# Optimization experiments

Hardware: AMD Instinct MI355X
Metric: run time of the kernel (lower is better)

The kernel has to match this reference:

```python
import jax, jax.numpy as jnp
import numpy as np

S, L, K = 4, 256, 32          # num_states, seq length, neighbors
ORIG_H, EMB_H, EXV, RANK = 128, 256, 384, 16


def _integrate(x, Wq, Wk, seq_idx, emb_idx, hidden, rank):
    """AttentionIntegrator.forward: QK^T softmax -> double mean -> softmax -> weighted pool of raw x."""
    x = jnp.moveaxis(x, (seq_idx, emb_idx), (-2, -1))
    orig_shape = x.shape
    Ls = orig_shape[-2]
    xf = x.reshape(-1, Ls, hidden)               # (B, Ls, hidden)
    B = xf.shape[0]
    q = (xf @ Wq.T).reshape(B, Ls, rank, hidden)  # head_dim == hidden
    k = (xf @ Wk.T).reshape(B, Ls, rank, hidden)
    scale = 1.0 / jnp.sqrt(jnp.asarray(hidden, xf.dtype))
    scores = jnp.einsum('blhd,bmhd->bhlm', q, k) * scale
    attn = jax.nn.softmax(scores, axis=-1)        # (B, rank, Ls, Ls)
    w = jax.nn.softmax(attn.mean(axis=(1, 2)), axis=-1)  # (B, Ls)
    pooled = jnp.einsum('bl,bld->bd', w, xf)      # (B, hidden)
    return (pooled.reshape(*orig_shape[:-2], hidden),
            w.reshape(*orig_shape[:-2], Ls))


def setup_inputs() -> dict:
    key = jax.random.key(0)
    ks = jax.random.split(key, 12)
    sc = lambda fan_in: 1.0 / np.sqrt(fan_in)
    return {
        'h_V':    jax.random.normal(ks[0], (S, L, ORIG_H), jnp.float32),
        'h_EXV':  jax.random.normal(ks[1], (S, L, K, EXV), jnp.float32),
        'W_hV':   jax.random.normal(ks[2], (EMB_H, ORIG_H), jnp.float32) * sc(ORIG_H),
        'b_hV':   jnp.zeros((EMB_H,), jnp.float32),
        'Wq_hv':  jax.random.normal(ks[3], (RANK * EMB_H, EMB_H), jnp.float32) * sc(EMB_H),
        'Wk_hv':  jax.random.normal(ks[4], (RANK * EMB_H, EMB_H), jnp.float32) * sc(EMB_H),
        'Wq_ce':  jax.random.normal(ks[5], (RANK * EXV, EXV), jnp.float32) * sc(EXV),
        'Wk_ce':  jax.random.normal(ks[6], (RANK * EXV, EXV), jnp.float32) * sc(EXV),
        'W_ce':   jax.random.normal(ks[7], (EMB_H, EXV), jnp.float32) * sc(EXV),
        'b_ce':   jnp.zeros((EMB_H,), jnp.float32),
        'Wq_sce': jax.random.normal(ks[8], (RANK * EMB_H, EMB_H), jnp.float32) * sc(EMB_H),
        'Wk_sce': jax.random.normal(ks[9], (RANK * EMB_H, EMB_H), jnp.float32) * sc(EMB_H),
    }


def reference(h_V, h_EXV, W_hV, b_hV, Wq_hv, Wk_hv, Wq_ce, Wk_ce, W_ce, b_ce, Wq_sce, Wk_sce):
    # diffmodel.get_weights
    hv = h_V @ W_hV.T + b_hV                                  # (S, L, EMB_H)
    h_V_int, h_V_w = _integrate(hv, Wq_hv, Wk_hv, 0, 2, EMB_H, RANK)   # pool over states
    # chemical environment: pool over k neighbors per (state, position)
    ce, _local_w = _integrate(h_EXV, Wq_ce, Wk_ce, 2, 3, EXV, RANK)    # (S, L, EXV)
    ce = ce @ W_ce.T + b_ce                                   # (S, L, EMB_H)
    ce_int, ce_w = _integrate(ce, Wq_sce, Wk_sce, 0, 2, EMB_H, RANK)   # pool over states
    return (h_V_int[None], h_V_w[None], ce_int[None], ce_w[None])
```

## Files before the change

kernel.cpp:

```cpp
#include <hip/hip_runtime.h>

typedef _Float16 f16;
typedef _Float16 f16x8 __attribute__((ext_vector_type(8)));
typedef _Float16 f16x4 __attribute__((ext_vector_type(4)));
typedef float f32x4 __attribute__((ext_vector_type(4)));

#define MFMA16(a, b, c) __builtin_amdgcn_mfma_f32_16x16x32_f16(a, b, c, 0, 0, 0)
#define MFMA16K16(a, b, c) __builtin_amdgcn_mfma_f32_16x16x16f16(a, b, c, 0, 0, 0)

__global__ __launch_bounds__(256) void k_mt(const float* __restrict__ Wq,
                                            const float* __restrict__ Wk,
                                            f16* __restrict__ MT, int H) {
    const int h = blockIdx.x;
    const int ntile = H >> 6;
    const int nkk = H >> 5;
    const int frow = (blockIdx.y / ntile) * 64;
    const int ecol = (blockIdx.y % ntile) * 64;
    const int t = threadIdx.x;
    const int lane = t & 63;
    const int w = t >> 6;
    const int wr = w >> 1, wc = w & 1;

    __shared__ __align__(16) f16 As[64][40];
    __shared__ __align__(16) f16 Ks[64][40];

    f32x4 acc[2][2] = {};
    const int d = t >> 3;
    const int e8 = (t & 7) * 8;

    for (int kk = 0; kk < nkk; ++kk) {
        const float* gq = Wq + (size_t)(h * H + kk * 32 + d) * H + ecol + e8;
        const float* gk = Wk + (size_t)(h * H + kk * 32 + d) * H + frow + e8;
        float q[8], k[8];
#pragma unroll
        for (int i = 0; i < 8; ++i) { q[i] = gq[i]; k[i] = gk[i]; }
        __syncthreads();
#pragma unroll
        for (int i = 0; i < 8; ++i) { As[e8 + i][d] = (f16)q[i]; Ks[e8 + i][d] = (f16)k[i]; }
        __syncthreads();
        f16x8 a[2], b[2];
#pragma unroll
        for (int rt = 0; rt < 2; ++rt)
            a[rt] = *(const f16x8*)&Ks[wr * 32 + rt * 16 + (lane & 15)][(lane >> 4) * 8];
#pragma unroll
        for (int nt = 0; nt < 2; ++nt)
            b[nt] = *(const f16x8*)&As[wc * 32 + nt * 16 + (lane & 15)][(lane >> 4) * 8];
#pragma unroll
        for (int rt = 0; rt < 2; ++rt)
#pragma unroll
            for (int nt = 0; nt < 2; ++nt)
                acc[rt][nt] = MFMA16(a[rt], b[nt], acc[rt][nt]);
    }
#pragma unroll
    for (int rt = 0; rt < 2; ++rt)
#pragma unroll
        for (int nt = 0; nt < 2; ++nt)
#pragma unroll
            for (int j = 0; j < 4; ++j) {
                int f = frow + wr * 32 + rt * 16 + (lane >> 4) * 4 + j;
                int e = ecol + wc * 32 + nt * 16 + (lane & 15);
                MT[(((size_t)h * nkk + (e >> 5)) * H + f) * 32 + (e & 31)] = (f16)acc[rt][nt][j];
            }
}

__global__ __launch_bounds__(256) void k_lin(const float* __restrict__ in,
                                             const float* __restrict__ W,
                                             const float* __restrict__ bias,
                                             float* __restrict__ out, int K) {
    const int t = threadIdx.x;
    const int r0 = blockIdx.x * 4;
    __shared__ float ins[4][384];
    __shared__ float Ws[256][33];
#pragma unroll
    for (int r = 0; r < 4; ++r)
        for (int off = t; off < K; off += 256)
            ins[r][off] = in[(size_t)(r0 + r) * K + off];
    float acc[4] = {};
    for (int d0 = 0; d0 < K; d0 += 32) {
        __syncthreads();
        for (int i = t; i < 256 * 32; i += 256) {
            int j = i >> 5, dd = i & 31;
            Ws[j][dd] = W[(size_t)j * K + d0 + dd];
        }
        __syncthreads();
#pragma unroll 8
        for (int dd = 0; dd < 32; ++dd) {
            float wv = Ws[t][dd];
#pragma unroll
            for (int r = 0; r < 4; ++r) acc[r] += wv * ins[r][d0 + dd];
        }
    }
    float bv = bias[t];
#pragma unroll
    for (int r = 0; r < 4; ++r) out[(size_t)(r0 + r) * 256 + t] = acc[r] + bv;
}

__global__ __launch_bounds__(256) void k_small_int(const float* __restrict__ X,
                                                   const f16* __restrict__ MT,
                                                   float* __restrict__ wpart) {
    const int t = threadIdx.x;
    const int lane = t & 63;
    const int w = t >> 6;
    const int g = lane >> 4;
    const int l15 = lane & 15;
    const int pos0 = blockIdx.x * 4;
    const int h = blockIdx.y;

    __shared__ __align__(16) f16 Xs[16][264];
    __shared__ __align__(16) f16 Ts[16][264];

    {
        int row = t >> 4, d0 = (t & 15) * 16;
        int s = row & 3, p = row >> 2;
        const float* gx = X + (size_t)(s * 256 + pos0 + p) * 256 + d0;
#pragma unroll
        for (int i = 0; i < 16; i += 8) {
            float4 v0 = *(const float4*)(gx + i);
            float4 v1 = *(const float4*)(gx + i + 4);
            f16x8 o;
            o[0] = (f16)v0.x; o[1] = (f16)v0.y; o[2] = (f16)v0.z; o[3] = (f16)v0.w;
            o[4] = (f16)v1.x; o[5] = (f16)v1.y; o[6] = (f16)v1.z; o[7] = (f16)v1.w;
            *(f16x8*)&Xs[row][d0 + i] = o;
        }
    }
    __syncthreads();

    const f16* mh = MT + (size_t)h * 8 * 256 * 32;
    const int fb = w * 64 + l15;
    f32x4 acc[4] = {};
    f16x8 bq[4], bn[4];
#pragma unroll
    for (int nt = 0; nt < 4; ++nt)
        bq[nt] = *(const f16x8*)(mh + (size_t)(fb + nt * 16) * 32 + g * 8);
#pragma unroll
    for (int kk = 0; kk < 8; ++kk) {
        if (kk < 7) {
#pragma unroll
            for (int nt = 0; nt < 4; ++nt)
                bn[nt] = *(const f16x8*)(mh + ((size_t)(kk + 1) * 256 + fb + nt * 16) * 32 + g * 8);
        }
        f16x8 a = *(const f16x8*)&Xs[l15][kk * 32 + g * 8];
#pragma unroll
        for (int nt = 0; nt < 4; ++nt) acc[nt] = MFMA16(a, bq[nt], acc[nt]);
#pragma unroll
        for (int nt = 0; nt < 4; ++nt) bq[nt] = bn[nt];
    }
#pragma unroll
    for (int nt = 0; nt < 4; ++nt)
#pragma unroll
        for (int j = 0; j < 4; ++j)
            Ts[g * 4 + j][w * 64 + nt * 16 + l15] = (f16)acc[nt][j];
    __syncthreads();

    f32x4 sacc = {};
#pragma unroll
    for (int ks = 0; ks < 8; ++ks) {
        f16x8 a = *(const f16x8*)&Ts[l15][ks * 32 + g * 8];
        f16x8 b = *(const f16x8*)&Xs[l15][ks * 32 + g * 8];
        sacc = MFMA16(a, b, sacc);
    }
    if (w == 0 && (l15 >> 2) == g) {
        const float scale = 1.0f / 16.0f;
        float add = 0.f;
#pragma unroll
        for (int j = 0; j < 4; ++j) {
            float v = sacc[j] * scale;
            float m = v;
            m = fmaxf(m, __shfl_xor(m, 1));
            m = fmaxf(m, __shfl_xor(m, 2));
            float e = expf(v - m);
            float s2 = e;
            s2 += __shfl_xor(s2, 1);
            s2 += __shfl_xor(s2, 2);
            add += e / s2;
        }
        int pg = pos0 + g;
        wpart[((size_t)h * 256 + pg) * 4 + (l15 & 3)] = add;
    }
}

__global__ __launch_bounds__(256) void k_small_fin(const float* __restrict__ wpart,
                                                   const float* __restrict__ X,
                                                   float* __restrict__ out_int,
                                                   float* __restrict__ out_w) {
    const int pos = blockIdx.x, t = threadIdx.x;
    __shared__ float red[64];
    __shared__ float ws[4];
    if (t < 64) red[t] = wpart[((size_t)(t >> 2) * 256 + pos) * 4 + (t & 3)];
    __syncthreads();
    if (t == 0) {
        float v[4];
#pragma unroll
        for (int s = 0; s < 4; ++s) {
            float x = 0.f;
            for (int hh = 0; hh < 16; ++hh) x += red[hh * 4 + s];
            v[s] = x * (1.0f / 64.0f);
        }
        float m = fmaxf(fmaxf(v[0], v[1]), fmaxf(v[2], v[3]));
        float sum = 0.f;
#pragma unroll
        for (int s = 0; s < 4; ++s) { v[s] = expf(v[s] - m); sum += v[s]; }
#pragma unroll
        for (int s = 0; s < 4; ++s) ws[s] = v[s] / sum;
    }
    __syncthreads();
    if (t < 4) out_w[pos * 4 + t] = ws[t];
    float v = 0.f;
#pragma unroll
    for (int s = 0; s < 4; ++s) v += ws[s] * X[(size_t)(s * 256 + pos) * 256 + t];
    out_int[(size_t)pos * 256 + t] = v;
}

#define PART_OFF 49152

__global__ __launch_bounds__(256, 2) void k_ce_int(const float* __restrict__ Xg32,
                                                   const f16* __restrict__ MT,
                                                   float* __restrict__ acc_out) {
    const int t = threadIdx.x;
    const int lane = t & 63;
    const int w = t >> 6;
    const int g = lane >> 4;
    const int l15 = lane & 15;
    const int bg = blockIdx.x;

    extern __shared__ __align__(16) char smem[];

    {
        const float* xg = Xg32 + (size_t)bg * 64 * 384;
#pragma unroll
        for (int p = 0; p < 12; ++p) {
            int idx = p * 256 + t;
            int row = idx / 48, s = idx - row * 48;
            int c = s ^ (row & 7);
            const float* src = xg + row * 384 + c * 8;
            float4 v0 = *(const float4*)src;
            float4 v1 = *(const float4*)(src + 4);
            f16x8 o;
            o[0] = (f16)v0.x; o[1] = (f16)v0.y; o[2] = (f16)v0.z; o[3] = (f16)v0.w;
            o[4] = (f16)v1.x; o[5] = (f16)v1.y; o[6] = (f16)v1.z; o[7] = (f16)v1.w;
            *(f16x8*)(smem + idx * 16) = o;
        }
    }
    __syncthreads();

    const f16* mall = MT;
    const int frow = w * 96 + l15;

    f16x8 A[3][6];
#pragma unroll
    for (int ft = 0; ft < 6; ++ft) {
        A[0][ft] = *(const f16x8*)(mall + ((size_t)0 * 384 + frow + ft * 16) * 32 + g * 8);
        A[1][ft] = *(const f16x8*)(mall + ((size_t)1 * 384 + frow + ft * 16) * 32 + g * 8);
    }

    for (int hi = 0; hi < 16; ++hi) {
        f32x4 acc[6][4] = {};
#pragma unroll
        for (int kk = 0; kk < 12; ++kk) {
            {
                int step = hi * 12 + kk + 2;
                int ns = step < 192 ? step : 191;
#pragma unroll
                for (int ft = 0; ft < 6; ++ft)
                    A[(kk + 2) % 3][ft] =
                        *(const f16x8*)(mall + ((size_t)ns * 384 + frow + ft * 16) * 32 + g * 8);
            }
            f16x8 xb[4];
#pragma unroll
            for (int mt = 0; mt < 4; ++mt) {
                int row = mt * 16 + l15;
                int ch = kk * 4 + g;
                xb[mt] = *(const f16x8*)(smem + row * 768 + ((ch ^ (row & 7)) << 4));
            }
            __builtin_amdgcn_s_setprio(1);
#pragma unroll
            for (int ft = 0; ft < 6; ++ft)
#pragma unroll
                for (int mt = 0; mt < 4; ++mt)
                    acc[ft][mt] = MFMA16(A[kk % 3][ft], xb[mt], acc[ft][mt]);
            __builtin_amdgcn_s_setprio(0);
        }

        f16x4 bf[6][4];
#pragma unroll
        for (int ft = 0; ft < 6; ++ft)
#pragma unroll
            for (int mt = 0; mt < 4; ++mt) {
                f32x4 v = acc[ft][mt];
                f16x4 o;
                o[0] = (f16)v[0]; o[1] = (f16)v[1]; o[2] = (f16)v[2]; o[3] = (f16)v[3];
                bf[ft][mt] = o;
            }

        f32x4 s2[2][2][2] = {};
#pragma unroll
        for (int b = 0; b < 2; ++b)
#pragma unroll
            for (int ks = 0; ks < 6; ++ks)
#pragma unroll
                for (int it = 0; it < 2; ++it) {
                    int r = b * 32 + it * 16 + l15;
                    int ch = 12 * w + 2 * ks + (g >> 1);
                    f16x4 av = *(const f16x4*)(smem + r * 768 + ((ch ^ (r & 7)) << 4) + 8 * (g & 1));
#pragma unroll
                    for (int lt = 0; lt < 2; ++lt)
                        s2[b][it][lt] = MFMA16K16(av, bf[ks][2 * b + lt], s2[b][it][lt]);
                }

#pragma unroll
        for (int b = 0; b < 2; ++b)
#pragma unroll
            for (int lt = 0; lt < 2; ++lt) {
                int dst = b * 2 + lt;
                if (dst != w) {
                    int src = w - (w > dst ? 1 : 0);
#pragma unroll
                    for (int it = 0; it < 2; ++it)
                        *(f32x4*)(smem + PART_OFF + (((dst * 3 + src) * 2 + it) << 10) + lane * 16) =
                            s2[b][it][lt];
                }
            }
        __syncthreads();

        {
            const int b = w >> 1, lt = w & 1;
            f32x4 own0, own1;
            if (w == 0)      { own0 = s2[0][0][0]; own1 = s2[0][1][0]; }
            else if (w == 1) { own0 = s2[0][0][1]; own1 = s2[0][1][1]; }
            else if (w == 2) { own0 = s2[1][0][0]; own1 = s2[1][1][0]; }
            else             { own0 = s2[1][0][1]; own1 = s2[1][1][1]; }
            f32x4 ssum[2] = { own0, own1 };
#pragma unroll
            for (int src = 0; src < 3; ++src)
#pragma unroll
                for (int it = 0; it < 2; ++it)
                    ssum[it] += *(const f32x4*)(smem + PART_OFF + (((w * 3 + src) * 2 + it) << 10) + lane * 16);

            const float scale = 0.051031036307982884f;
            float mx = -1e30f;
#pragma unroll
            for (int it = 0; it < 2; ++it)
#pragma unroll
                for (int j = 0; j < 4; ++j) mx = fmaxf(mx, ssum[it][j] * scale);
            mx = fmaxf(mx, __shfl_xor(mx, 16));
            mx = fmaxf(mx, __shfl_xor(mx, 32));
            float e[2][4];
            float den = 0.f;
#pragma unroll
            for (int it = 0; it < 2; ++it)
#pragma unroll
                for (int j = 0; j < 4; ++j) {
                    e[it][j] = expf(ssum[it][j] * scale - mx);
                    den += e[it][j];
                }
            den += __shfl_xor(den, 16);
            den += __shfl_xor(den, 32);
            float inv = 1.f / den;
            float cs[2][4];
#pragma unroll
            for (int it = 0; it < 2; ++it)
#pragma unroll
                for (int j = 0; j < 4; ++j) {
                    float v = e[it][j] * inv;
                    v += __shfl_xor(v, 1);
                    v += __shfl_xor(v, 2);
                    v += __shfl_xor(v, 4);
                    v += __shfl_xor(v, 8);
                    cs[it][j] = v;
                }
            if (l15 == 0) {
                float* o = acc_out + (((size_t)hi * 1024 + bg * 2 + b) * 2 + lt) * 32;
#pragma unroll
                for (int it = 0; it < 2; ++it)
#pragma unroll
                    for (int j = 0; j < 4; ++j)
                        o[it * 16 + g * 4 + j] = cs[it][j];
            }
        }
        __syncthreads();
    }
}

__global__ __launch_bounds__(128) void k_ce_pool(const float* __restrict__ accp,
                                                 const float* __restrict__ exv,
                                                 float* __restrict__ pooled) {
    const int b = blockIdx.x;
    const int t = threadIdx.x;
    __shared__ float wm[32];
    __shared__ float ww[32];
    if (t < 32) {
        float s = 0.f;
#pragma unroll
        for (int h = 0; h < 16; ++h) {
            s += accp[(((size_t)h * 1024 + b) * 2 + 0) * 32 + t];
            s += accp[(((size_t)h * 1024 + b) * 2 + 1) * 32 + t];
        }
        wm[t] = s * (1.0f / 512.0f);
    }
    __syncthreads();
    if (t == 0) {
        float m = wm[0];
        for (int i = 1; i < 32; ++i) m = fmaxf(m, wm[i]);
        float s = 0.f;
        for (int i = 0; i < 32; ++i) { float e = expf(wm[i] - m); ww[i] = e; s += e; }
        float inv = 1.f / s;
        for (int i = 0; i < 32; ++i) ww[i] *= inv;
    }
    __syncthreads();
    for (int d = t; d < 384; d += 128) {
        float v = 0.f;
#pragma unroll
        for (int m = 0; m < 32; ++m) v += ww[m] * exv[((size_t)b * 32 + m) * 384 + d];
        pooled[(size_t)b * 384 + d] = v;
    }
}

extern "C" void kernel_launch(void* const* d_in, const int* in_sizes, int n_in,
                              void* d_out, int out_size, void* d_ws, size_t ws_size,
                              hipStream_t stream) {
    const float* h_V    = (const float*)d_in[0];
    const float* h_EXV  = (const float*)d_in[1];
    const float* W_hV   = (const float*)d_in[2];
    const float* b_hV   = (const float*)d_in[3];
    const float* Wq_hv  = (const float*)d_in[4];
    const float* Wk_hv  = (const float*)d_in[5];
    const float* Wq_ce  = (const float*)d_in[6];
    const float* Wk_ce  = (const float*)d_in[7];
    const float* W_ce   = (const float*)d_in[8];
    const float* b_ce   = (const float*)d_in[9];
    const float* Wq_sce = (const float*)d_in[10];
    const float* Wk_sce = (const float*)d_in[11];
    float* out = (float*)d_out;

    char* ws = (char*)d_ws;
    f16*   mt_hv  = (f16*)(ws + 0);
    f16*   mt_sce = (f16*)(ws + 2097152);
    f16*   mt_ce  = (f16*)(ws + 4194304);
    float* hv     = (float*)(ws + 8912896);
    float* ce     = (float*)(ws + 9961472);
    float* accp   = (float*)(ws + 11010048);
    float* pooled = (float*)(ws + 15204352);
    float* wpart  = accp;

    k_mt<<<dim3(16, 16), 256, 0, stream>>>(Wq_hv, Wk_hv, mt_hv, 256);
    k_mt<<<dim3(16, 36), 256, 0, stream>>>(Wq_ce, Wk_ce, mt_ce, 384);
    k_mt<<<dim3(16, 16), 256, 0, stream>>>(Wq_sce, Wk_sce, mt_sce, 256);
    k_lin<<<256, 256, 0, stream>>>(h_V, W_hV, b_hV, hv, 128);
    k_small_int<<<dim3(64, 16), 256, 0, stream>>>(hv, mt_hv, wpart);
    k_small_fin<<<256, 256, 0, stream>>>(wpart, hv, out + 0, out + 65536);
    k_ce_int<<<dim3(512), 256, 73728, stream>>>(h_EXV, mt_ce, accp);
    k_ce_pool<<<1024, 128, 0, stream>>>(accp, h_EXV, pooled);
    k_lin<<<256, 256, 0, stream>>>(pooled, W_ce, b_ce, ce, 384);
    k_small_int<<<dim3(64, 16), 256, 0, stream>>>(ce, mt_sce, wpart);
    k_small_fin<<<256, 256, 0, stream>>>(wpart, ce, out + 66560, out + 132096);
}
```

Baseline: 315.3 us.

## Split k_ce_int work across eight waves with tree reduction of score partials

The main neighbor-attention kernel now runs 512 threads per block instead of 256. Each wave handles 48 feature rows instead of 96, and the MT prefetch ring shrinks from triple to double buffering, which lowers per-wave register pressure and raises waves in flight. The cross-wave reduction of score partials becomes a staged pairwise exchange through shared memory, and the softmax reductions are split across wave pairs. This adds many more __syncthreads per head iteration, and the shorter prefetch distance may expose global load latency.

Measured after the change: 351.9 us. +11.6%, slower.

```diff
diff --git a/kernel.cpp b/kernel.cpp
--- a/kernel.cpp
+++ b/kernel.cpp
@@ -211,9 +211,9 @@
     out_int[(size_t)pos * 256 + t] = v;
 }
 
-#define PART_OFF 49152
-
-__global__ __launch_bounds__(256, 2) void k_ce_int(const float* __restrict__ Xg32,
+#define EX_OFF 49152
+
+__global__ __launch_bounds__(512, 2) void k_ce_int(const float* __restrict__ Xg32,
                                                    const f16* __restrict__ MT,
                                                    float* __restrict__ acc_out) {
     const int t = threadIdx.x;
@@ -224,12 +224,13 @@
     const int bg = blockIdx.x;
 
     extern __shared__ __align__(16) char smem[];
+    char* EX = smem + EX_OFF;
 
     {
         const float* xg = Xg32 + (size_t)bg * 64 * 384;
 #pragma unroll
-        for (int p = 0; p < 12; ++p) {
-            int idx = p * 256 + t;
+        for (int p = 0; p < 6; ++p) {
+            int idx = p * 512 + t;
             int row = idx / 48, s = idx - row * 48;
             int c = s ^ (row & 7);
             const float* src = xg + row * 384 + c * 8;
@@ -244,46 +245,42 @@
     __syncthreads();
 
     const f16* mall = MT;
-    const int frow = w * 96 + l15;
-
-    f16x8 A[3][6];
-#pragma unroll
-    for (int ft = 0; ft < 6; ++ft) {
-        A[0][ft] = *(const f16x8*)(mall + ((size_t)0 * 384 + frow + ft * 16) * 32 + g * 8);
-        A[1][ft] = *(const f16x8*)(mall + ((size_t)1 * 384 + frow + ft * 16) * 32 + g * 8);
-    }
+    const int frow = w * 48 + l15;
+
+    f16x8 A[2][3];
+#pragma unroll
+    for (int ft = 0; ft < 3; ++ft)
+        A[0][ft] = *(const f16x8*)(mall + (size_t)(frow + ft * 16) * 32 + g * 8);
 
     for (int hi = 0; hi < 16; ++hi) {
-        f32x4 acc[6][4] = {};
+        f32x4 acc[3][4] = {};
 #pragma unroll
         for (int kk = 0; kk < 12; ++kk) {
             {
-                int step = hi * 12 + kk + 2;
+                int step = hi * 12 + kk + 1;
                 int ns = step < 192 ? step : 191;
 #pragma unroll
-                for (int ft = 0; ft < 6; ++ft)
-                    A[(kk + 2) % 3][ft] =
-                        *(const f16x8*)(mall + ((size_t)ns * 384 + frow + ft * 16) * 32 + g * 8);
+                for (int ft = 0; ft < 3; ++ft)
+                    A[(kk + 1) & 1][ft] =
+                        *(const f16x8*)(mall + (size_t)ns * 12288 + (size_t)(frow + ft * 16) * 32 + g * 8);
             }
+            const int xaddr = l15 * 768 + (((kk * 4 + g) ^ (l15 & 7)) << 4);
             f16x8 xb[4];
 #pragma unroll
-            for (int mt = 0; mt < 4; ++mt) {
-                int row = mt * 16 + l15;
-                int ch = kk * 4 + g;
-                xb[mt] = *(const f16x8*)(smem + row * 768 + ((ch ^ (row & 7)) << 4));
-            }
+            for (int mt = 0; mt < 4; ++mt)
+                xb[mt] = *(const f16x8*)(smem + xaddr + mt * 12288);
             __builtin_amdgcn_s_setprio(1);
 #pragma unroll
-            for (int ft = 0; ft < 6; ++ft)
+            for (int ft = 0; ft < 3; ++ft)
 #pragma unroll
                 for (int mt = 0; mt < 4; ++mt)
-                    acc[ft][mt] = MFMA16(A[kk % 3][ft], xb[mt], acc[ft][mt]);
+                    acc[ft][mt] = MFMA16(A[kk & 1][ft], xb[mt], acc[ft][mt]);
             __builtin_amdgcn_s_setprio(0);
         }
 
-        f16x4 bf[6][4];
-#pragma unroll
-        for (int ft = 0; ft < 6; ++ft)
+        f16x4 bf[3][4];
+#pragma unroll
+        for (int ft = 0; ft < 3; ++ft)
 #pragma unroll
             for (int mt = 0; mt < 4; ++mt) {
                 f32x4 v = acc[ft][mt];
@@ -296,85 +293,109 @@
 #pragma unroll
         for (int b = 0; b < 2; ++b)
 #pragma unroll
-            for (int ks = 0; ks < 6; ++ks)
+            for (int ks = 0; ks < 3; ++ks)
 #pragma unroll
                 for (int it = 0; it < 2; ++it) {
-                    int r = b * 32 + it * 16 + l15;
-                    int ch = 12 * w + 2 * ks + (g >> 1);
-                    f16x4 av = *(const f16x4*)(smem + r * 768 + ((ch ^ (r & 7)) << 4) + 8 * (g & 1));
+                    int ch = 6 * w + 2 * ks + (g >> 1);
+                    int av_addr = b * 24576 + it * 12288 + l15 * 768 +
+                                  ((ch ^ (l15 & 7)) << 4) + 8 * (g & 1);
+                    f16x4 av = *(const f16x4*)(smem + av_addr);
 #pragma unroll
                     for (int lt = 0; lt < 2; ++lt)
-                        s2[b][it][lt] = MFMA16K16(av, bf[ks][2 * b + lt], s2[b][it][lt]);
+                        s2[b][it][lt] = MFMA16K16(av, bf[ks][b * 2 + lt], s2[b][it][lt]);
                 }
 
-#pragma unroll
-        for (int b = 0; b < 2; ++b)
-#pragma unroll
-            for (int lt = 0; lt < 2; ++lt) {
-                int dst = b * 2 + lt;
-                if (dst != w) {
-                    int src = w - (w > dst ? 1 : 0);
-#pragma unroll
-                    for (int it = 0; it < 2; ++it)
-                        *(f32x4*)(smem + PART_OFF + (((dst * 3 + src) * 2 + it) << 10) + lane * 16) =
-                            s2[b][it][lt];
-                }
+        f32x4 p00, p01, p10, p11;
+        if (w >= 4) {
+            char* dst = EX + (w - 4) * 4096 + lane * 16;
+            *(f32x4*)(dst) = s2[0][0][0];
+            *(f32x4*)(dst + 1024) = s2[0][0][1];
+            *(f32x4*)(dst + 2048) = s2[0][1][0];
+            *(f32x4*)(dst + 3072) = s2[0][1][1];
+        }
+        __syncthreads();
+        if (w < 4) {
+            const char* pb = EX + w * 4096 + lane * 16;
+            p00 = s2[0][0][0] + *(const f32x4*)(pb);
+            p01 = s2[0][0][1] + *(const f32x4*)(pb + 1024);
+            p10 = s2[0][1][0] + *(const f32x4*)(pb + 2048);
+            p11 = s2[0][1][1] + *(const f32x4*)(pb + 3072);
+            char* dst = EX + w * 4096 + lane * 16;
+            *(f32x4*)(dst) = s2[1][0][0];
+            *(f32x4*)(dst + 1024) = s2[1][0][1];
+            *(f32x4*)(dst + 2048) = s2[1][1][0];
+            *(f32x4*)(dst + 3072) = s2[1][1][1];
+        }
+        __syncthreads();
+        if (w >= 4) {
+            const char* pb = EX + (w - 4) * 4096 + lane * 16;
+            p00 = s2[1][0][0] + *(const f32x4*)(pb);
+            p01 = s2[1][0][1] + *(const f32x4*)(pb + 1024);
+            p10 = s2[1][1][0] + *(const f32x4*)(pb + 2048);
+            p11 = s2[1][1][1] + *(const f32x4*)(pb + 3072);
+        }
+        __syncthreads();
+
+        {
+            char* dst = EX + w * 2048 + lane * 16;
+            if ((w & 2) == 0) { *(f32x4*)dst = p10; *(f32x4*)(dst + 1024) = p11; }
+            else              { *(f32x4*)dst = p00; *(f32x4*)(dst + 1024) = p01; }
+        }
+        __syncthreads();
+        f32x4 q0, q1;
+        {
+            const char* pb = EX + (w ^ 2) * 2048 + lane * 16;
+            if ((w & 2) == 0) { q0 = p00 + *(const f32x4*)pb; q1 = p01 + *(const f32x4*)(pb + 1024); }
+            else              { q0 = p10 + *(const f32x4*)pb; q1 = p11 + *(const f32x4*)(pb + 1024); }
+        }
+        __syncthreads();
+
+        {
+            char* dst = EX + w * 1024 + lane * 16;
+            if ((w & 1) == 0) *(f32x4*)dst = q1;
+            else              *(f32x4*)dst = q0;
+        }
+        __syncthreads();
+        f32x4 fin;
+        {
+            const char* pb = EX + (w ^ 1) * 1024 + lane * 16;
+            if ((w & 1) == 0) fin = q0 + *(const f32x4*)pb;
+            else              fin = q1 + *(const f32x4*)pb;
+        }
+        __syncthreads();
+
+        {
+            const float scale = 0.051031036307982884f;
+            float v0 = fin[0] * scale, v1 = fin[1] * scale;
+            float v2 = fin[2] * scale, v3 = fin[3] * scale;
+            float lm = fmaxf(fmaxf(v0, v1), fmaxf(v2, v3));
+            lm = fmaxf(lm, __shfl_xor(lm, 16));
+            lm = fmaxf(lm, __shfl_xor(lm, 32));
+            if (lane < 16) *(float*)(EX + w * 64 + lane * 4) = lm;
+            __syncthreads();
+            float m = fmaxf(lm, *(const float*)(EX + (w ^ 2) * 64 + l15 * 4));
+            float e0 = expf(v0 - m), e1 = expf(v1 - m);
+            float e2 = expf(v2 - m), e3 = expf(v3 - m);
+            float ls = e0 + e1 + e2 + e3;
+            ls += __shfl_xor(ls, 16);
+            ls += __shfl_xor(ls, 32);
+            if (lane < 16) *(float*)(EX + 512 + w * 64 + lane * 4) = ls;
+            __syncthreads();
+            float den = ls + *(const float*)(EX + 512 + (w ^ 2) * 64 + l15 * 4);
+            float inv = 1.f / den;
+            float r0 = e0 * inv, r1 = e1 * inv, r2 = e2 * inv, r3 = e3 * inv;
+#pragma unroll
+            for (int d = 1; d < 16; d <<= 1) {
+                r0 += __shfl_xor(r0, d);
+                r1 += __shfl_xor(r1, d);
+                r2 += __shfl_xor(r2, d);
+                r3 += __shfl_xor(r3, d);
             }
-        __syncthreads();
-
-        {
-            const int b = w >> 1, lt = w & 1;
-            f32x4 own0, own1;
-            if (w == 0)      { own0 = s2[0][0][0]; own1 = s2[0][1][0]; }
-            else if (w == 1) { own0 = s2[0][0][1]; own1 = s2[0][1][1]; }
-            else if (w == 2) { own0 = s2[1][0][0]; own1 = s2[1][1][0]; }
-            else             { own0 = s2[1][0][1]; own1 = s2[1][1][1]; }
-            f32x4 ssum[2] = { own0, own1 };
-#pragma unroll
-            for (int src = 0; src < 3; ++src)
-#pragma unroll
-                for (int it = 0; it < 2; ++it)
-                    ssum[it] += *(const f32x4*)(smem + PART_OFF + (((w * 3 + src) * 2 + it) << 10) + lane * 16);
-
-            const float scale = 0.051031036307982884f;
-            float mx = -1e30f;
-#pragma unroll
-            for (int it = 0; it < 2; ++it)
-#pragma unroll
-                for (int j = 0; j < 4; ++j) mx = fmaxf(mx, ssum[it][j] * scale);
-            mx = fmaxf(mx, __shfl_xor(mx, 16));
-            mx = fmaxf(mx, __shfl_xor(mx, 32));
-            float e[2][4];
-            float den = 0.f;
-#pragma unroll
-            for (int it = 0; it < 2; ++it)
-#pragma unroll
-                for (int j = 0; j < 4; ++j) {
-                    e[it][j] = expf(ssum[it][j] * scale - mx);
-                    den += e[it][j];
-                }
-            den += __shfl_xor(den, 16);
-            den += __shfl_xor(den, 32);
-            float inv = 1.f / den;
-            float cs[2][4];
-#pragma unroll
-            for (int it = 0; it < 2; ++it)
-#pragma unroll
-                for (int j = 0; j < 4; ++j) {
-                    float v = e[it][j] * inv;
-                    v += __shfl_xor(v, 1);
-                    v += __shfl_xor(v, 2);
-                    v += __shfl_xor(v, 4);
-                    v += __shfl_xor(v, 8);
-                    cs[it][j] = v;
-                }
             if (l15 == 0) {
-                float* o = acc_out + (((size_t)hi * 1024 + bg * 2 + b) * 2 + lt) * 32;
-#pragma unroll
-                for (int it = 0; it < 2; ++it)
-#pragma unroll
-                    for (int j = 0; j < 4; ++j)
-                        o[it * 16 + g * 4 + j] = cs[it][j];
+                const int ob = w >> 2, oit = (w >> 1) & 1, olt = w & 1;
+                float* o = acc_out + (((size_t)hi * 1024 + bg * 2 + ob) * 2 + olt) * 32 +
+                           oit * 16 + g * 4;
+                o[0] = r0; o[1] = r1; o[2] = r2; o[3] = r3;
             }
         }
         __syncthreads();
@@ -448,7 +469,7 @@
     k_lin<<<256, 256, 0, stream>>>(h_V, W_hV, b_hV, hv, 128);
     k_small_int<<<dim3(64, 16), 256, 0, stream>>>(hv, mt_hv, wpart);
     k_small_fin<<<256, 256, 0, stream>>>(wpart, hv, out + 0, out + 65536);
-    k_ce_int<<<dim3(512), 256, 73728, stream>>>(h_EXV, mt_ce, accp);
+    k_ce_int<<<dim3(512), 512, 65536, stream>>>(h_EXV, mt_ce, accp);
     k_ce_pool<<<1024, 128, 0, stream>>>(accp, h_EXV, pooled);
     k_lin<<<256, 256, 0, stream>>>(pooled, W_ce, b_ce, ce, 384);
     k_small_int<<<dim3(64, 16), 256, 0, stream>>>(ce, mt_sce, wpart);
```

## Double rows per block in ce integrator to halve per-row weight fetches

Applied to the files above, without the earlier changes.

k_ce_int now uses 512-thread blocks that each process 128 neighbor rows instead of 64. Each of 8 waves covers 48 feature rows of the combined Q/K matrix against 8 row tiles, so each fetched weight fragment is reused across twice as many rows and global/L2 traffic for MT drops. The cross-wave score reduction moves to a 64KB LDS buffer and runs in two rounds, each with a synchronisation, where four waves reduce and compute the softmax. The 160KB LDS footprint allows only one block per CU, and the larger register tiles may reduce occupancy.

New measurement: 318.7 us. About the same (+1.1%).

```diff
diff --git a/kernel.cpp b/kernel.cpp
--- a/kernel.cpp
+++ b/kernel.cpp
@@ -211,9 +211,9 @@
     out_int[(size_t)pos * 256 + t] = v;
 }
 
-#define PART_OFF 49152
-
-__global__ __launch_bounds__(256, 2) void k_ce_int(const float* __restrict__ Xg32,
+#define BUF_OFF 98304
+
+__global__ __launch_bounds__(512, 2) void k_ce_int(const float* __restrict__ Xg32,
                                                    const f16* __restrict__ MT,
                                                    float* __restrict__ acc_out) {
     const int t = threadIdx.x;
@@ -224,12 +224,13 @@
     const int bg = blockIdx.x;
 
     extern __shared__ __align__(16) char smem[];
+    char* BUF = smem + BUF_OFF;
 
     {
-        const float* xg = Xg32 + (size_t)bg * 64 * 384;
+        const float* xg = Xg32 + (size_t)bg * 128 * 384;
 #pragma unroll
         for (int p = 0; p < 12; ++p) {
-            int idx = p * 256 + t;
+            int idx = p * 512 + t;
             int row = idx / 48, s = idx - row * 48;
             int c = s ^ (row & 7);
             const float* src = xg + row * 384 + c * 8;
@@ -244,140 +245,126 @@
     __syncthreads();
 
     const f16* mall = MT;
-    const int frow = w * 96 + l15;
-
-    f16x8 A[3][6];
-#pragma unroll
-    for (int ft = 0; ft < 6; ++ft) {
-        A[0][ft] = *(const f16x8*)(mall + ((size_t)0 * 384 + frow + ft * 16) * 32 + g * 8);
-        A[1][ft] = *(const f16x8*)(mall + ((size_t)1 * 384 + frow + ft * 16) * 32 + g * 8);
+    const int frow = w * 48 + l15;
+
+    f16x8 A[3][3];
+#pragma unroll
+    for (int ft = 0; ft < 3; ++ft) {
+        A[0][ft] = *(const f16x8*)(mall + (size_t)(frow + ft * 16) * 32 + g * 8);
+        A[1][ft] = *(const f16x8*)(mall + (size_t)12288 + (size_t)(frow + ft * 16) * 32 + g * 8);
     }
 
     for (int hi = 0; hi < 16; ++hi) {
-        f32x4 acc[6][4] = {};
+        f32x4 acc[3][8] = {};
 #pragma unroll
         for (int kk = 0; kk < 12; ++kk) {
             {
                 int step = hi * 12 + kk + 2;
                 int ns = step < 192 ? step : 191;
 #pragma unroll
-                for (int ft = 0; ft < 6; ++ft)
+                for (int ft = 0; ft < 3; ++ft)
                     A[(kk + 2) % 3][ft] =
-                        *(const f16x8*)(mall + ((size_t)ns * 384 + frow + ft * 16) * 32 + g * 8);
-            }
-            f16x8 xb[4];
-#pragma unroll
-            for (int mt = 0; mt < 4; ++mt) {
+                        *(const f16x8*)(mall + (size_t)ns * 12288 + (size_t)(frow + ft * 16) * 32 + g * 8);
+            }
+            f16x8 xb[8];
+#pragma unroll
+            for (int mt = 0; mt < 8; ++mt) {
                 int row = mt * 16 + l15;
                 int ch = kk * 4 + g;
                 xb[mt] = *(const f16x8*)(smem + row * 768 + ((ch ^ (row & 7)) << 4));
             }
             __builtin_amdgcn_s_setprio(1);
 #pragma unroll
-            for (int ft = 0; ft < 6; ++ft)
-#pragma unroll
-                for (int mt = 0; mt < 4; ++mt)
+            for (int ft = 0; ft < 3; ++ft)
+#pragma unroll
+                for (int mt = 0; mt < 8; ++mt)
                     acc[ft][mt] = MFMA16(A[kk % 3][ft], xb[mt], acc[ft][mt]);
             __builtin_amdgcn_s_setprio(0);
         }
 
-        f16x4 bf[6][4];
-#pragma unroll
-        for (int ft = 0; ft < 6; ++ft)
-#pragma unroll
-            for (int mt = 0; mt < 4; ++mt) {
+        f16x4 bf[3][8];
+#pragma unroll
+        for (int ft = 0; ft < 3; ++ft)
+#pragma unroll
+            for (int mt = 0; mt < 8; ++mt) {
                 f32x4 v = acc[ft][mt];
                 f16x4 o;
                 o[0] = (f16)v[0]; o[1] = (f16)v[1]; o[2] = (f16)v[2]; o[3] = (f16)v[3];
                 bf[ft][mt] = o;
             }
 
-        f32x4 s2[2][2][2] = {};
-#pragma unroll
-        for (int b = 0; b < 2; ++b)
-#pragma unroll
-            for (int ks = 0; ks < 6; ++ks)
-#pragma unroll
-                for (int it = 0; it < 2; ++it) {
-                    int r = b * 32 + it * 16 + l15;
-                    int ch = 12 * w + 2 * ks + (g >> 1);
-                    f16x4 av = *(const f16x4*)(smem + r * 768 + ((ch ^ (r & 7)) << 4) + 8 * (g & 1));
+#pragma unroll
+        for (int r = 0; r < 2; ++r) {
+            f32x4 s2[2][2][2] = {};
+#pragma unroll
+            for (int bb = 0; bb < 2; ++bb) {
+                const int b = 2 * r + bb;
+#pragma unroll
+                for (int ks = 0; ks < 3; ++ks)
+#pragma unroll
+                    for (int it = 0; it < 2; ++it) {
+                        int row = b * 32 + it * 16 + l15;
+                        int ch = 6 * w + 2 * ks + (g >> 1);
+                        f16x4 av = *(const f16x4*)(smem + row * 768 +
+                                                   ((ch ^ (row & 7)) << 4) + 8 * (g & 1));
+#pragma unroll
+                        for (int lt = 0; lt < 2; ++lt)
+                            s2[bb][it][lt] = MFMA16K16(av, bf[ks][2 * b + lt], s2[bb][it][lt]);
+                    }
+            }
+#pragma unroll
+            for (int bb = 0; bb < 2; ++bb)
+#pragma unroll
+                for (int it = 0; it < 2; ++it)
 #pragma unroll
                     for (int lt = 0; lt < 2; ++lt)
-                        s2[b][it][lt] = MFMA16K16(av, bf[ks][2 * b + lt], s2[b][it][lt]);
+                        *(f32x4*)(BUF + w * 8192 + (bb * 4 + it * 2 + lt) * 1024 + lane * 16) =
+                            s2[bb][it][lt];
+            __syncthreads();
+
+            if ((w >> 2) == r) {
+                const int wl = w & 3;
+                const int bb = wl >> 1;
+                const int it = wl & 1;
+                const int b = 2 * r + bb;
+                f32x4 sum0 = {0.f, 0.f, 0.f, 0.f};
+                f32x4 sum1 = {0.f, 0.f, 0.f, 0.f};
+#pragma unroll
+                for (int src = 0; src < 8; ++src) {
+                    const char* pb = BUF + src * 8192 + (bb * 4 + it * 2) * 1024 + lane * 16;
+                    sum0 += *(const f32x4*)pb;
+                    sum1 += *(const f32x4*)(pb + 1024);
                 }
-
-#pragma unroll
-        for (int b = 0; b < 2; ++b)
-#pragma unroll
-            for (int lt = 0; lt < 2; ++lt) {
-                int dst = b * 2 + lt;
-                if (dst != w) {
-                    int src = w - (w > dst ? 1 : 0);
-#pragma unroll
-                    for (int it = 0; it < 2; ++it)
-                        *(f32x4*)(smem + PART_OFF + (((dst * 3 + src) * 2 + it) << 10) + lane * 16) =
-                            s2[b][it][lt];
+                const float scale = 0.051031036307982884f;
+                float cs0 = 0.f, cs1 = 0.f;
+#pragma unroll
+                for (int j = 0; j < 4; ++j) {
+                    float v0 = sum0[j] * scale, v1 = sum1[j] * scale;
+                    float m = fmaxf(v0, v1);
+                    m = fmaxf(m, __shfl_xor(m, 1));
+                    m = fmaxf(m, __shfl_xor(m, 2));
+                    m = fmaxf(m, __shfl_xor(m, 4));
+                    m = fmaxf(m, __shfl_xor(m, 8));
+                    float e0 = expf(v0 - m), e1 = expf(v1 - m);
+                    float s = e0 + e1;
+                    s += __shfl_xor(s, 1);
+                    s += __shfl_xor(s, 2);
+                    s += __shfl_xor(s, 4);
+                    s += __shfl_xor(s, 8);
+                    float inv = 1.f / s;
+                    cs0 += e0 * inv;
+                    cs1 += e1 * inv;
                 }
-            }
-        __syncthreads();
-
-        {
-            const int b = w >> 1, lt = w & 1;
-            f32x4 own0, own1;
-            if (w == 0)      { own0 = s2[0][0][0]; own1 = s2[0][1][0]; }
-            else if (w == 1) { own0 = s2[0][0][1]; own1 = s2[0][1][1]; }
-            else if (w == 2) { own0 = s2[1][0][0]; own1 = s2[1][1][0]; }
-            else             { own0 = s2[1][0][1]; own1 = s2[1][1][1]; }
-            f32x4 ssum[2] = { own0, own1 };
-#pragma unroll
-            for (int src = 0; src < 3; ++src)
-#pragma unroll
-                for (int it = 0; it < 2; ++it)
-                    ssum[it] += *(const f32x4*)(smem + PART_OFF + (((w * 3 + src) * 2 + it) << 10) + lane * 16);
-
-            const float scale = 0.051031036307982884f;
-            float mx = -1e30f;
-#pragma unroll
-            for (int it = 0; it < 2; ++it)
-#pragma unroll
-                for (int j = 0; j < 4; ++j) mx = fmaxf(mx, ssum[it][j] * scale);
-            mx = fmaxf(mx, __shfl_xor(mx, 16));
-            mx = fmaxf(mx, __shfl_xor(mx, 32));
-            float e[2][4];
-            float den = 0.f;
-#pragma unroll
-            for (int it = 0; it < 2; ++it)
-#pragma unroll
-                for (int j = 0; j < 4; ++j) {
-                    e[it][j] = expf(ssum[it][j] * scale - mx);
-                    den += e[it][j];
+                cs0 += __shfl_xor(cs0, 16); cs0 += __shfl_xor(cs0, 32);
+                cs1 += __shfl_xor(cs1, 16); cs1 += __shfl_xor(cs1, 32);
+                if (lane < 16) {
+                    float* o = acc_out + (((size_t)hi * 1024 + bg * 4 + b) * 2 + it) * 32;
+                    o[l15] = cs0;
+                    o[16 + l15] = cs1;
                 }
-            den += __shfl_xor(den, 16);
-            den += __shfl_xor(den, 32);
-            float inv = 1.f / den;
-            float cs[2][4];
-#pragma unroll
-            for (int it = 0; it < 2; ++it)
-#pragma unroll
-                for (int j = 0; j < 4; ++j) {
-                    float v = e[it][j] * inv;
-                    v += __shfl_xor(v, 1);
-                    v += __shfl_xor(v, 2);
-                    v += __shfl_xor(v, 4);
-                    v += __shfl_xor(v, 8);
-                    cs[it][j] = v;
-                }
-            if (l15 == 0) {
-                float* o = acc_out + (((size_t)hi * 1024 + bg * 2 + b) * 2 + lt) * 32;
-#pragma unroll
-                for (int it = 0; it < 2; ++it)
-#pragma unroll
-                    for (int j = 0; j < 4; ++j)
-                        o[it * 16 + g * 4 + j] = cs[it][j];
-            }
-        }
-        __syncthreads();
+            }
+            __syncthreads();
+        }
     }
 }
 
@@ -448,7 +435,7 @@
     k_lin<<<256, 256, 0, stream>>>(h_V, W_hV, b_hV, hv, 128);
     k_small_int<<<dim3(64, 16), 256, 0, stream>>>(hv, mt_hv, wpart);
     k_small_fin<<<256, 256, 0, stream>>>(wpart, hv, out + 0, out + 65536);
-    k_ce_int<<<dim3(512), 256, 73728, stream>>>(h_EXV, mt_ce, accp);
+    k_ce_int<<<dim3(256), 512, 163840, stream>>>(h_EXV, mt_ce, accp);
     k_ce_pool<<<1024, 128, 0, stream>>>(accp, h_EXV, pooled);
     k_lin<<<256, 256, 0, stream>>>(pooled, W_ce, b_ce, ce, 384);
     k_small_int<<<dim3(64, 16), 256, 0, stream>>>(ce, mt_sce, wpart);
```
